# Kernel tuning notes

Hardware: AMD Instinct MI355X
Metric: run time of the kernel (lower is better)

## Reference

```python
import jax, jax.numpy as jnp
import numpy as np

B, T, C = 2, 2048, 2048
N_HEAD, N_KV = 16, 4
HEAD_DIM = C // N_HEAD  # 128
ROPE_THETA = 10000.0


def setup_inputs() -> dict:
    key = jax.random.key(0)
    ks = jax.random.split(key, 5)
    x = jax.random.normal(ks[0], (B, T, C), dtype=jnp.float32)
    # rope frequencies: cos/sin of pos * theta^(-2i/d), shape [T, HEAD_DIM//2, 2]
    inv_freq = 1.0 / (ROPE_THETA ** (jnp.arange(0, HEAD_DIM, 2, dtype=jnp.float32) / HEAD_DIM))
    angles = jnp.arange(T, dtype=jnp.float32)[:, None] * inv_freq[None, :]  # [T, D/2]
    rope_freqs = jnp.stack([jnp.cos(angles), jnp.sin(angles)], axis=-1)  # [T, D/2, 2]
    std = 0.02
    wq = jax.random.normal(ks[1], (C, C), dtype=jnp.float32) * std            # q: Linear(C, C)
    wkv = jax.random.normal(ks[2], (2 * N_KV * HEAD_DIM, C), dtype=jnp.float32) * std  # kv: Linear(C, 2*Hkv*D)
    wo = jax.random.normal(ks[3], (C, C), dtype=jnp.float32) * std
    bo = jax.random.normal(ks[4], (C,), dtype=jnp.float32) * std
    return {"x": x, "rope_freqs": rope_freqs, "wq": wq, "wkv": wkv, "wo": wo, "bo": bo}


def _apply_rope(t, cos, sin):
    # t: [B, H, T, D]; cos/sin: [T, D/2] -> complex rotation on (even, odd) pairs
    tr = t.reshape(*t.shape[:-1], -1, 2)  # [B, H, T, D/2, 2]
    t0, t1 = tr[..., 0], tr[..., 1]
    c = cos[None, None, :, :]
    s = sin[None, None, :, :]
    r0 = t0 * c - t1 * s
    r1 = t0 * s + t1 * c
    return jnp.stack([r0, r1], axis=-1).reshape(t.shape)


def reference(x, rope_freqs, wq, wkv, wo, bo):
    Bx, Tx, Cx = x.shape
    D = HEAD_DIM
    prop = N_HEAD // N_KV
    q = (x @ wq.T).reshape(Bx, Tx, N_HEAD, D).transpose(0, 2, 1, 3)  # [B, H, T, D]
    kv = x @ wkv.T
    k, v = jnp.split(kv, 2, axis=-1)
    k = k.reshape(Bx, Tx, N_KV, D).transpose(0, 2, 1, 3)  # [B, Hkv, T, D]
    v = v.reshape(Bx, Tx, N_KV, D).transpose(0, 2, 1, 3)
    cos, sin = rope_freqs[..., 0], rope_freqs[..., 1]
    q = _apply_rope(q, cos, sin)
    k = _apply_rope(k, cos, sin)
    # torch .repeat tiles: query head h -> kv head (h % N_KV)
    k = jnp.tile(k, (1, prop, 1, 1))  # [B, H, T, D]
    v = jnp.tile(v, (1, prop, 1, 1))
    scale = 1.0 / jnp.sqrt(jnp.float32(D))
    scores = jnp.einsum('bhtd,bhsd->bhts', q, k) * scale  # [B, H, T, T]
    causal = jnp.tril(jnp.ones((Tx, Tx), dtype=bool))
    scores = jnp.where(causal[None, None], scores, jnp.finfo(scores.dtype).min)
    attn = jax.nn.softmax(scores, axis=-1)
    out = jnp.einsum('bhts,bhsd->bhtd', attn, v)  # [B, H, T, D]
    out = out.transpose(0, 2, 1, 3).reshape(Bx, Tx, Cx)
    return out @ wo.T + bo
```

## Files before the change

### kernel.cpp

```cpp
#include <hip/hip_runtime.h>
#include <hip/hip_bf16.h>
#include <stdint.h>

#define B_ 2
#define T_ 2048
#define C_ 2048
#define NH 16
#define NKV 4
#define HD 128

typedef __attribute__((ext_vector_type(4))) float f32x4;
typedef __attribute__((ext_vector_type(8))) short bf16x8;
typedef __attribute__((ext_vector_type(4))) int i32x4;

static __device__ __forceinline__ ushort f2bf(float f) {
  return __bfloat16_as_ushort(__float2bfloat16(f));
}
static __device__ __forceinline__ uint32_t pack_bf(float a, float b) {
  return (uint32_t)f2bf(a) | ((uint32_t)f2bf(b) << 16);
}

typedef __attribute__((address_space(1))) const void g1void;
typedef __attribute__((address_space(3))) void l3void;
static __device__ __forceinline__ void gload16(const void* g, void* l) {
  __builtin_amdgcn_global_load_lds((g1void*)g, (l3void*)l, 16, 0, 0);
}

__global__ __launch_bounds__(256)
void cast_bf16(const float* __restrict__ in, ushort* __restrict__ out, int n4) {
  for (int i = blockIdx.x * 256 + threadIdx.x; i < n4; i += gridDim.x * 256) {
    float4 v = ((const float4*)in)[i];
    ushort4 o;
    o.x = f2bf(v.x); o.y = f2bf(v.y); o.z = f2bf(v.z); o.w = f2bf(v.w);
    ((ushort4*)out)[i] = o;
  }
}

template<int MODE>
__global__ __launch_bounds__(256)
void gemm_mfma(const ushort* __restrict__ A, const ushort* __restrict__ W,
               const float* __restrict__ bias, float* __restrict__ Cf,
               ushort* __restrict__ O1, ushort* __restrict__ O2,
               const float* __restrict__ rf, int M, int N, int K) {
  __shared__ __align__(16) ushort As[128 * 64];
  __shared__ __align__(16) ushort Ws[128 * 64];
  const int tid = threadIdx.x;
  const int lane = tid & 63, wid = tid >> 6;
  const int wr = wid >> 1, wc = wid & 1;
  const int lr = lane & 15, lg = lane >> 4;
  const int bm = blockIdx.y * 128, bn = blockIdx.x * 128;

  f32x4 acc[4][4];
  #pragma unroll
  for (int mi = 0; mi < 4; ++mi)
    #pragma unroll
    for (int nj = 0; nj < 4; ++nj) acc[mi][nj] = f32x4{0.f, 0.f, 0.f, 0.f};

  const ushort* Ab = A + (size_t)bm * K;
  const ushort* Wb = W + (size_t)bn * K;

  for (int k0 = 0; k0 < K; k0 += 64) {
    #pragma unroll
    for (int it = 0; it < 4; ++it) {
      const int cid = it * 256 + tid;
      const int r = cid >> 3, cc = (cid & 7) * 8;
      gload16(Ab + (size_t)r * K + k0 + cc, &As[cid * 8]);
      gload16(Wb + (size_t)r * K + k0 + cc, &Ws[cid * 8]);
    }
    __syncthreads();
    #pragma unroll
    for (int ks = 0; ks < 2; ++ks) {
      bf16x8 af[4], bf[4];
      #pragma unroll
      for (int i = 0; i < 4; ++i) {
        af[i] = *(const bf16x8*)&As[(wr * 64 + i * 16 + lr) * 64 + ks * 32 + lg * 8];
        bf[i] = *(const bf16x8*)&Ws[(wc * 64 + i * 16 + lr) * 64 + ks * 32 + lg * 8];
      }
      #pragma unroll
      for (int mi = 0; mi < 4; ++mi)
        #pragma unroll
        for (int nj = 0; nj < 4; ++nj)
          acc[mi][nj] = __builtin_amdgcn_mfma_f32_16x16x32_bf16(af[mi], bf[nj], acc[mi][nj], 0, 0, 0);
    }
    __syncthreads();
  }
  #pragma unroll
  for (int nj = 0; nj < 4; ++nj) {
    const int cn = bn + wc * 64 + nj * 16 + lr;
    const float bv = (MODE == 0) ? bias[cn] : 0.0f;
    #pragma unroll
    for (int mi = 0; mi < 4; ++mi) {
      const int rm = bm + wr * 64 + mi * 16 + lg * 4;
      #pragma unroll
      for (int r = 0; r < 4; ++r) {
        const int row = rm + r;
        const float v = acc[mi][nj][r];
        if (MODE == 0) {
          Cf[(size_t)row * N + cn] = v + bv;
        } else {
          const int t = row & (T_ - 1), bb = row >> 11;
          if (MODE == 2 && cn >= 512) {
            O2[(size_t)row * 512 + (cn - 512)] = f2bf(v);
          } else {
            const int d = cn & 127;
            const float2 cs = *(const float2*)&rf[t * HD + (d & ~1)];
            const float p = __shfl_xor(v, 1);
            float o = (cn & 1) ? (p * cs.y + v * cs.x) : (v * cs.x - p * cs.y);
            if (MODE == 1) {
              o *= 0.08838834764831845f;
              O1[(((size_t)(bb * NH + (cn >> 7))) * T_ + t) * HD + d] = f2bf(o);
            } else {
              O1[(((size_t)(bb * NKV + (cn >> 7))) * T_ + t) * HD + d] = f2bf(o);
            }
          }
        }
      }
    }
  }
}

__global__ __launch_bounds__(256)
void v_transpose(const ushort* __restrict__ Vtmp, ushort* __restrict__ Vt) {
  __shared__ ushort tl[64][65];
  const int bt = blockIdx.x;
  const int bc = blockIdx.y;
  const int tid = threadIdx.x;
  for (int i = tid; i < 64 * 16; i += 256) {
    const int tr = i >> 4, c4 = i & 15;
    ushort4 v = *(const ushort4*)&Vtmp[(size_t)(bt * 64 + tr) * 512 + bc * 64 + c4 * 4];
    tl[tr][c4 * 4 + 0] = v.x; tl[tr][c4 * 4 + 1] = v.y;
    tl[tr][c4 * 4 + 2] = v.z; tl[tr][c4 * 4 + 3] = v.w;
  }
  __syncthreads();
  const int b = bt >> 5, tloc0 = (bt * 64) & (T_ - 1);
  const int g = (bc * 64) >> 7, dbase = (bc * 64) & 127;
  for (int i = tid; i < 64 * 16; i += 256) {
    const int dr = i >> 4, t4 = i & 15;
    ushort4 v;
    v.x = tl[t4 * 4 + 0][dr]; v.y = tl[t4 * 4 + 1][dr];
    v.z = tl[t4 * 4 + 2][dr]; v.w = tl[t4 * 4 + 3][dr];
    *(ushort4*)&Vt[(((size_t)(b * NKV + g)) * HD + dbase + dr) * T_ + tloc0 + t4 * 4] = v;
  }
}

__global__ __launch_bounds__(512, 4)
void flash_attn(const ushort* __restrict__ Qb, const ushort* __restrict__ Kb,
                const ushort* __restrict__ Vt, ushort* __restrict__ ATb) {
  __shared__ __align__(16) ushort Ks[2][64 * 128];
  __shared__ __align__(16) ushort Vs[2][128 * 64];

  const int f = blockIdx.x;
  const int second = f >> 8;
  const int fb = f & 255;
  const int bxl = fb & 15;
  const int bh = (fb >> 4) + (second << 4);
  const int qstrip = second ? bxl : (15 - bxl);
  const int q0 = qstrip * 128;

  const int b = bh >> 4, h = bh & 15, g = h & (NKV - 1);
  const int tid = threadIdx.x;
  const int wid = tid >> 6;
  const int lane = tid & 63;
  const int lg = lane >> 4;
  const int qi = lane & 15;
  const int qrow = q0 + wid * 16 + qi;
  const int swz = (qi & 7) << 4;

  const ushort* Qw = Qb + (((size_t)(b * NH + h)) * T_ + qrow) * HD;
  bf16x8 qf[4];
  #pragma unroll
  for (int dsl = 0; dsl < 4; ++dsl)
    qf[dsl] = *(const bf16x8*)(Qw + dsl * 32 + lg * 8);

  const ushort* Kbase = Kb + ((size_t)(b * NKV + g)) * T_ * HD;
  const ushort* Vbase = Vt + ((size_t)(b * NKV + g)) * HD * T_;

  float m = -3.0e38f, l = 0.f;
  f32x4 oacc[8];
  #pragma unroll
  for (int i = 0; i < 8; ++i) oacc[i] = f32x4{0.f, 0.f, 0.f, 0.f};

  const int nkv = 2 * qstrip + 2;

  auto stage = [&](int buf, int sblk) {
    #pragma unroll
    for (int it = 0; it < 2; ++it) {
      const int c = it * 512 + tid;
      {
        const int r = c >> 4, o = (c & 15) * 16;
        gload16(Kbase + (size_t)(sblk + r) * HD + ((o ^ ((r & 7) << 4)) >> 1),
                &Ks[buf][c * 8]);
      }
      {
        const int d = c >> 3, o = (c & 7) * 16;
        gload16(Vbase + (size_t)d * T_ + sblk + ((o ^ ((d & 7) << 4)) >> 1),
                &Vs[buf][c * 8]);
      }
    }
  };

  auto compute = [&](int buf, int kv) {
    const int sblk = kv * 64;
    f32x4 sacc[4];
    #pragma unroll
    for (int st = 0; st < 4; ++st) sacc[st] = f32x4{0.f, 0.f, 0.f, 0.f};
    #pragma unroll
    for (int st = 0; st < 4; ++st) {
      const ushort* kr = &Ks[buf][(st * 16 + qi) * 128];
      #pragma unroll
      for (int dsl = 0; dsl < 4; ++dsl) {
        bf16x8 kf = *(const bf16x8*)(kr + (((dsl * 64 + lg * 16) ^ swz) >> 1));
        sacc[st] = __builtin_amdgcn_mfma_f32_16x16x32_bf16(kf, qf[dsl], sacc[st], 0, 0, 0);
      }
    }
    float sc[16];
    #pragma unroll
    for (int st = 0; st < 4; ++st)
      #pragma unroll
      for (int r = 0; r < 4; ++r) sc[st * 4 + r] = sacc[st][r];
    if (kv >= nkv - 2) {
      #pragma unroll
      for (int st = 0; st < 4; ++st)
        #pragma unroll
        for (int r = 0; r < 4; ++r) {
          const int s = sblk + st * 16 + lg * 4 + r;
          if (s > qrow) sc[st * 4 + r] = -3.0e38f;
        }
    }
    float mt = sc[0];
    #pragma unroll
    for (int i = 1; i < 16; ++i) mt = fmaxf(mt, sc[i]);
    mt = fmaxf(mt, __shfl_xor(mt, 16));
    mt = fmaxf(mt, __shfl_xor(mt, 32));
    if (!__all(mt - m <= 8.0f)) {
      const float mn = fmaxf(m, mt);
      const float alpha = __expf(m - mn);
      l *= alpha;
      #pragma unroll
      for (int i = 0; i < 8; ++i) oacc[i] *= alpha;
      m = mn;
    }
    float ps = 0.f;
    #pragma unroll
    for (int i = 0; i < 16; ++i) { sc[i] = __expf(sc[i] - m); ps += sc[i]; }
    ps += __shfl_xor(ps, 16);
    ps += __shfl_xor(ps, 32);
    l += ps;
    uint32_t wtw[4][2];
    #pragma unroll
    for (int t = 0; t < 4; ++t) {
      wtw[t][0] = pack_bf(sc[4 * t + 0], sc[4 * t + 1]);
      wtw[t][1] = pack_bf(sc[4 * t + 2], sc[4 * t + 3]);
    }
    bf16x8 pfrag[2];
    #pragma unroll
    for (int ss = 0; ss < 2; ++ss) {
      int w[4];
      #pragma unroll
      for (int v = 0; v < 4; ++v) {
        const int addr = ((2 * (lg & 1) + (v >> 1)) * 16 + qi) * 4;
        const int r0 = __builtin_amdgcn_ds_bpermute(addr, (int)wtw[2 * ss][v & 1]);
        const int r1 = __builtin_amdgcn_ds_bpermute(addr, (int)wtw[2 * ss + 1][v & 1]);
        w[v] = (lg & 2) ? r1 : r0;
      }
      i32x4 tmp = {w[0], w[1], w[2], w[3]};
      pfrag[ss] = __builtin_bit_cast(bf16x8, tmp);
    }
    #pragma unroll
    for (int dt = 0; dt < 8; ++dt) {
      const ushort* vr = &Vs[buf][(dt * 16 + qi) * 64];
      const bf16x8 v0 = *(const bf16x8*)(vr + (((lg * 16) ^ swz) >> 1));
      const bf16x8 v1 = *(const bf16x8*)(vr + (((64 + lg * 16) ^ swz) >> 1));
      oacc[dt] = __builtin_amdgcn_mfma_f32_16x16x32_bf16(v0, pfrag[0], oacc[dt], 0, 0, 0);
      oacc[dt] = __builtin_amdgcn_mfma_f32_16x16x32_bf16(v1, pfrag[1], oacc[dt], 0, 0, 0);
    }
  };

  stage(0, 0);
  __syncthreads();
  for (int kv = 0; kv < nkv - 1; ++kv) {
    stage((kv + 1) & 1, (kv + 1) * 64);
    compute(kv & 1, kv);
    __syncthreads();
  }
  compute((nkv - 1) & 1, nkv - 1);

  const float inv = 1.0f / l;
  ushort* orow = ATb + ((size_t)(b * T_) + qrow) * C_ + h * HD;
  #pragma unroll
  for (int dt = 0; dt < 8; ++dt) {
    f32x4 o = oacc[dt] * inv;
    ushort4 ob;
    ob.x = f2bf(o[0]); ob.y = f2bf(o[1]); ob.z = f2bf(o[2]); ob.w = f2bf(o[3]);
    *(ushort4*)(orow + dt * 16 + lg * 4) = ob;
  }
}

extern "C" void kernel_launch(void* const* d_in, const int* in_sizes, int n_in,
                              void* d_out, int out_size, void* d_ws, size_t ws_size,
                              hipStream_t stream) {
  const float* x   = (const float*)d_in[0];
  const float* rf  = (const float*)d_in[1];
  const float* wq  = (const float*)d_in[2];
  const float* wkv = (const float*)d_in[3];
  const float* wo  = (const float*)d_in[4];
  const float* bo  = (const float*)d_in[5];
  float* out = (float*)d_out;

  uint8_t* w = (uint8_t*)d_ws;
  ushort* ATb  = (ushort*)w;  w += (size_t)4096 * 2048 * 2;
  ushort* Vtmp = (ushort*)w;  w += (size_t)4096 * 512 * 2;
  ushort* Qb   = (ushort*)w;  w += (size_t)4096 * 2048 * 2;
  ushort* Kb   = (ushort*)w;  w += (size_t)4096 * 512 * 2;
  ushort* Vt   = (ushort*)w;  w += (size_t)4096 * 512 * 2;
  ushort* xb   = (ushort*)w;  w += (size_t)4096 * 2048 * 2;
  ushort* wqb  = (ushort*)w;  w += (size_t)2048 * 2048 * 2;
  ushort* wkvb = (ushort*)w;  w += (size_t)1024 * 2048 * 2;
  ushort* wob  = (ushort*)w;  w += (size_t)2048 * 2048 * 2;

  dim3 blk(256);
  cast_bf16<<<dim3(2048), blk, 0, stream>>>(x,   xb,   4096 * 2048 / 4);
  cast_bf16<<<dim3(2048), blk, 0, stream>>>(wq,  wqb,  2048 * 2048 / 4);
  cast_bf16<<<dim3(1024), blk, 0, stream>>>(wkv, wkvb, 1024 * 2048 / 4);
  cast_bf16<<<dim3(2048), blk, 0, stream>>>(wo,  wob,  2048 * 2048 / 4);

  gemm_mfma<1><<<dim3(16, 32), blk, 0, stream>>>(xb, wqb, nullptr, nullptr,
                                                 Qb, nullptr, rf, 4096, 2048, 2048);
  gemm_mfma<2><<<dim3(8, 32), blk, 0, stream>>>(xb, wkvb, nullptr, nullptr,
                                                Kb, Vtmp, rf, 4096, 1024, 2048);
  v_transpose<<<dim3(64, 8), blk, 0, stream>>>(Vtmp, Vt);
  flash_attn<<<dim3(512), dim3(512), 0, stream>>>(Qb, Kb, Vt, ATb);
  gemm_mfma<0><<<dim3(16, 32), blk, 0, stream>>>(ATb, wob, bo, out,
                                                 nullptr, nullptr, nullptr, 4096, 2048, 2048);
}
```

Baseline: 254.2 us.

## Fuse QKV projections into one GEMM, write V transposed, merge cast kernels

Concatenates wq and wkv into a single bf16 weight buffer so Q, K and V come from one 4096x3072 GEMM launch instead of two. The epilogue writes V directly in the transposed [b,g,d,t] layout as 4-wide vectors, which removes the separate v_transpose kernel and its intermediate buffer. The four cast launches are merged into one kernel that splits its blocks across tensors. This cuts launch count and intermediate traffic and gives a larger, better-filled grid. The cost is branchier epilogue code and strided transposed stores for V.

```diff
diff --git a/kernel.cpp b/kernel.cpp
--- a/kernel.cpp
+++ b/kernel.cpp
@@ -27,12 +27,22 @@
 }
 
 __global__ __launch_bounds__(256)
-void cast_bf16(const float* __restrict__ in, ushort* __restrict__ out, int n4) {
-  for (int i = blockIdx.x * 256 + threadIdx.x; i < n4; i += gridDim.x * 256) {
-    float4 v = ((const float4*)in)[i];
+void cast_all(const float* __restrict__ x, const float* __restrict__ wq,
+              const float* __restrict__ wkv, const float* __restrict__ wo,
+              ushort* __restrict__ xb, ushort* __restrict__ wqkvb,
+              ushort* __restrict__ wob) {
+  const int bid = blockIdx.x;
+  const float* src; ushort* dst; int n4, b0, nblk;
+  if (bid < 1024)      { src = x;   dst = xb;    n4 = 2097152; b0 = 0;    nblk = 1024; }
+  else if (bid < 1536) { src = wq;  dst = wqkvb; n4 = 1048576; b0 = 1024; nblk = 512; }
+  else if (bid < 1792) { src = wkv; dst = wqkvb + (size_t)2048 * 2048;
+                         n4 = 524288;  b0 = 1536; nblk = 256; }
+  else                 { src = wo;  dst = wob;   n4 = 1048576; b0 = 1792; nblk = 512; }
+  for (int i = (bid - b0) * 256 + threadIdx.x; i < n4; i += nblk * 256) {
+    float4 v = ((const float4*)src)[i];
     ushort4 o;
     o.x = f2bf(v.x); o.y = f2bf(v.y); o.z = f2bf(v.z); o.w = f2bf(v.w);
-    ((ushort4*)out)[i] = o;
+    ((ushort4*)dst)[i] = o;
   }
 }
 
@@ -41,6 +51,7 @@
 void gemm_mfma(const ushort* __restrict__ A, const ushort* __restrict__ W,
                const float* __restrict__ bias, float* __restrict__ Cf,
                ushort* __restrict__ O1, ushort* __restrict__ O2,
+               ushort* __restrict__ O3,
                const float* __restrict__ rf, int M, int N, int K) {
   __shared__ __align__(16) ushort As[128 * 64];
   __shared__ __align__(16) ushort Ws[128 * 64];
@@ -91,55 +102,38 @@
     #pragma unroll
     for (int mi = 0; mi < 4; ++mi) {
       const int rm = bm + wr * 64 + mi * 16 + lg * 4;
-      #pragma unroll
-      for (int r = 0; r < 4; ++r) {
-        const int row = rm + r;
-        const float v = acc[mi][nj][r];
-        if (MODE == 0) {
-          Cf[(size_t)row * N + cn] = v + bv;
+      const int bb = rm >> 11, tl = rm & (T_ - 1);
+      if (MODE == 0) {
+        #pragma unroll
+        for (int r = 0; r < 4; ++r)
+          Cf[(size_t)(rm + r) * N + cn] = acc[mi][nj][r] + bv;
+      } else {
+        if (cn >= 2560) {
+          const int c = cn - 2560, gg = c >> 7, d = c & 127;
+          ushort4 ov;
+          ov.x = f2bf(acc[mi][nj][0]); ov.y = f2bf(acc[mi][nj][1]);
+          ov.z = f2bf(acc[mi][nj][2]); ov.w = f2bf(acc[mi][nj][3]);
+          *(ushort4*)&O2[(((size_t)(bb * NKV + gg)) * HD + d) * T_ + tl] = ov;
         } else {
-          const int t = row & (T_ - 1), bb = row >> 11;
-          if (MODE == 2 && cn >= 512) {
-            O2[(size_t)row * 512 + (cn - 512)] = f2bf(v);
-          } else {
-            const int d = cn & 127;
+          const int d = cn & 127;
+          #pragma unroll
+          for (int r = 0; r < 4; ++r) {
+            const int t = tl + r;
+            const float v = acc[mi][nj][r];
             const float2 cs = *(const float2*)&rf[t * HD + (d & ~1)];
             const float p = __shfl_xor(v, 1);
             float o = (cn & 1) ? (p * cs.y + v * cs.x) : (v * cs.x - p * cs.y);
-            if (MODE == 1) {
+            if (cn < 2048) {
               o *= 0.08838834764831845f;
               O1[(((size_t)(bb * NH + (cn >> 7))) * T_ + t) * HD + d] = f2bf(o);
             } else {
-              O1[(((size_t)(bb * NKV + (cn >> 7))) * T_ + t) * HD + d] = f2bf(o);
+              const int c = cn - 2048;
+              O3[(((size_t)(bb * NKV + (c >> 7))) * T_ + t) * HD + d] = f2bf(o);
             }
           }
         }
       }
     }
-  }
-}
-
-__global__ __launch_bounds__(256)
-void v_transpose(const ushort* __restrict__ Vtmp, ushort* __restrict__ Vt) {
-  __shared__ ushort tl[64][65];
-  const int bt = blockIdx.x;
-  const int bc = blockIdx.y;
-  const int tid = threadIdx.x;
-  for (int i = tid; i < 64 * 16; i += 256) {
-    const int tr = i >> 4, c4 = i & 15;
-    ushort4 v = *(const ushort4*)&Vtmp[(size_t)(bt * 64 + tr) * 512 + bc * 64 + c4 * 4];
-    tl[tr][c4 * 4 + 0] = v.x; tl[tr][c4 * 4 + 1] = v.y;
-    tl[tr][c4 * 4 + 2] = v.z; tl[tr][c4 * 4 + 3] = v.w;
-  }
-  __syncthreads();
-  const int b = bt >> 5, tloc0 = (bt * 64) & (T_ - 1);
-  const int g = (bc * 64) >> 7, dbase = (bc * 64) & 127;
-  for (int i = tid; i < 64 * 16; i += 256) {
-    const int dr = i >> 4, t4 = i & 15;
-    ushort4 v;
-    v.x = tl[t4 * 4 + 0][dr]; v.y = tl[t4 * 4 + 1][dr];
-    v.z = tl[t4 * 4 + 2][dr]; v.w = tl[t4 * 4 + 3][dr];
-    *(ushort4*)&Vt[(((size_t)(b * NKV + g)) * HD + dbase + dr) * T_ + tloc0 + t4 * 4] = v;
   }
 }
 
@@ -308,28 +302,20 @@
   float* out = (float*)d_out;
 
   uint8_t* w = (uint8_t*)d_ws;
-  ushort* ATb  = (ushort*)w;  w += (size_t)4096 * 2048 * 2;
-  ushort* Vtmp = (ushort*)w;  w += (size_t)4096 * 512 * 2;
-  ushort* Qb   = (ushort*)w;  w += (size_t)4096 * 2048 * 2;
-  ushort* Kb   = (ushort*)w;  w += (size_t)4096 * 512 * 2;
-  ushort* Vt   = (ushort*)w;  w += (size_t)4096 * 512 * 2;
-  ushort* xb   = (ushort*)w;  w += (size_t)4096 * 2048 * 2;
-  ushort* wqb  = (ushort*)w;  w += (size_t)2048 * 2048 * 2;
-  ushort* wkvb = (ushort*)w;  w += (size_t)1024 * 2048 * 2;
-  ushort* wob  = (ushort*)w;  w += (size_t)2048 * 2048 * 2;
+  ushort* ATb   = (ushort*)w;  w += (size_t)4096 * 2048 * 2;
+  ushort* Qb    = (ushort*)w;  w += (size_t)4096 * 2048 * 2;
+  ushort* Kb    = (ushort*)w;  w += (size_t)4096 * 512 * 2;
+  ushort* Vt    = (ushort*)w;  w += (size_t)4096 * 512 * 2;
+  ushort* xb    = (ushort*)w;  w += (size_t)4096 * 2048 * 2;
+  ushort* wqkvb = (ushort*)w;  w += (size_t)3072 * 2048 * 2;
+  ushort* wob   = (ushort*)w;  w += (size_t)2048 * 2048 * 2;
 
   dim3 blk(256);
-  cast_bf16<<<dim3(2048), blk, 0, stream>>>(x,   xb,   4096 * 2048 / 4);
-  cast_bf16<<<dim3(2048), blk, 0, stream>>>(wq,  wqb,  2048 * 2048 / 4);
-  cast_bf16<<<dim3(1024), blk, 0, stream>>>(wkv, wkvb, 1024 * 2048 / 4);
-  cast_bf16<<<dim3(2048), blk, 0, stream>>>(wo,  wob,  2048 * 2048 / 4);
-
-  gemm_mfma<1><<<dim3(16, 32), blk, 0, stream>>>(xb, wqb, nullptr, nullptr,
-                                                 Qb, nullptr, rf, 4096, 2048, 2048);
-  gemm_mfma<2><<<dim3(8, 32), blk, 0, stream>>>(xb, wkvb, nullptr, nullptr,
-                                                Kb, Vtmp, rf, 4096, 1024, 2048);
-  v_transpose<<<dim3(64, 8), blk, 0, stream>>>(Vtmp, Vt);
+  cast_all<<<dim3(2304), blk, 0, stream>>>(x, wq, wkv, wo, xb, wqkvb, wob);
+
+  gemm_mfma<3><<<dim3(24, 32), blk, 0, stream>>>(xb, wqkvb, nullptr, nullptr,
+                                                 Qb, Vt, Kb, rf, 4096, 3072, 2048);
   flash_attn<<<dim3(512), dim3(512), 0, stream>>>(Qb, Kb, Vt, ATb);
   gemm_mfma<0><<<dim3(16, 32), blk, 0, stream>>>(ATb, wob, bo, out,
-                                                 nullptr, nullptr, nullptr, 4096, 2048, 2048);
-}
+                                                 nullptr, nullptr, nullptr, nullptr, 4096, 2048, 2048);
+}
```

Result: faster. 240.7 us (-5.3%).
